# Performance work log

Measured on AMD Instinct MI355X. Metric: run time of the kernel, lower is better.

The kernel has to match this reference:

```python
import jax, jax.numpy as jnp
import numpy as np

N, E, NC, ES, NT, G = 200000, 500000, 150000, 350000, 100000, 1024
FN, FE, H, T = 133, 14, 128, 3


def _enc_params(key, prefix):
    ks = jax.random.split(key, 4)
    g = lambda k, shape, fan_in: jax.random.normal(k, shape, jnp.float32) / np.sqrt(fan_in).astype(np.float32)
    return {
        f"{prefix}_w_node": g(ks[0], (FN, H), FN),
        f"{prefix}_b_node": jnp.zeros((H,), jnp.float32),
        f"{prefix}_w_edge": g(ks[1], (FE, H), FE),
        f"{prefix}_b_edge": jnp.zeros((H,), jnp.float32),
        f"{prefix}_w_mp": g(ks[2], (T, H, H), H),
        f"{prefix}_b_mp": jnp.zeros((T, H), jnp.float32),
        f"{prefix}_w_out": g(ks[3], (H, H), H),
        f"{prefix}_b_out": jnp.zeros((H,), jnp.float32),
    }


def setup_inputs() -> dict:
    key = jax.random.key(0)
    k = lambda i: jax.random.fold_in(key, i)
    inp = {
        "x": jax.random.normal(k(0), (N, FN), jnp.float32),
        "node_weight": jax.random.uniform(k(1), (N,), jnp.float32),
        "edge_index": jax.random.randint(k(2), (2, E), 0, N),
        "edge_attr": jax.random.normal(k(3), (E, FE), jnp.float32),
        "edge_weight": jax.random.uniform(k(4), (E,), jnp.float32),
        "batch": jnp.sort(jax.random.randint(k(5), (N,), 0, G)),
        "context_nodes_mapper": jax.random.randint(k(6), (NC,), 0, N),
        "target_nodes_mapper": jax.random.randint(k(7), (NT,), 0, N),
        "combined_subgraphs": jax.random.randint(k(8), (2, ES), 0, NC),
        "subgraphs_edges_mapper": jax.random.randint(k(9), (ES,), 0, E),
        "context_edges_mask": jax.random.bernoulli(k(10), 0.7, (ES,)),
    }
    inp.update(_enc_params(k(11), "ctx"))
    inp.update(_enc_params(k(12), "tgt"))
    return inp


def wd_mpnn(x, src, dst, edge_attr, edge_weight, node_weight,
            w_node, b_node, w_edge, b_edge, w_mp, b_mp, w_out, b_out, n_nodes):
    # Weighted-edge node MPNN: gather source node states, combine with edge
    # embedding, scale by edge weight, scatter-sum onto destination nodes.
    h = jax.nn.relu(x @ w_node + b_node)                 # [n_nodes, H]
    eh = jax.nn.relu(edge_attr @ w_edge + b_edge)        # [n_edges, H]
    ew = edge_weight[:, None]
    for t in range(w_mp.shape[0]):
        msg = ew * (h[src] + eh)                         # gather [n_edges, H]
        agg = jax.ops.segment_sum(msg, dst, num_segments=n_nodes)
        h = jax.nn.relu(h + agg @ w_mp[t] + b_mp[t])
    return (h @ w_out + b_out) * node_weight[:, None]


def segment_mean(vals, seg, num_segments):
    s = jax.ops.segment_sum(vals, seg, num_segments=num_segments)
    c = jax.ops.segment_sum(jnp.ones((vals.shape[0],), vals.dtype), seg, num_segments=num_segments)
    return s / jnp.maximum(c, 1.0)[:, None]


def reference(x, node_weight, edge_index, edge_attr, edge_weight, batch,
              context_nodes_mapper, target_nodes_mapper, combined_subgraphs,
              subgraphs_edges_mapper, context_edges_mask,
              ctx_w_node, ctx_b_node, ctx_w_edge, ctx_b_edge, ctx_w_mp, ctx_b_mp, ctx_w_out, ctx_b_out,
              tgt_w_node, tgt_b_node, tgt_w_edge, tgt_b_edge, tgt_w_mp, tgt_b_mp, tgt_w_out, tgt_b_out):
    # --- context branch: gather subgraph node/edge features ---
    cx = x[context_nodes_mapper]                         # [NC, FN]
    cnw = node_weight[context_nodes_mapper]              # [NC]
    cea = edge_attr[subgraphs_edges_mapper]              # [ES, FE]
    # boolean edge mask folded into edge weights (messages scale linearly in
    # edge_weight, so zeroing masked edges == dropping them) -> jit friendly
    cew = edge_weight[subgraphs_edges_mapper] * context_edges_mask.astype(jnp.float32)
    csrc, cdst = combined_subgraphs[0], combined_subgraphs[1]
    ctx_nodes = wd_mpnn(cx, csrc, cdst, cea, cew, cnw,
                        ctx_w_node, ctx_b_node, ctx_w_edge, ctx_b_edge,
                        ctx_w_mp, ctx_b_mp, ctx_w_out, ctx_b_out, NC)
    ctx_emb = segment_mean(ctx_nodes, batch[context_nodes_mapper], G)   # [G, H]

    # --- target branch: full-graph encode, pool over target nodes ---
    full = wd_mpnn(x, edge_index[0], edge_index[1], edge_attr, edge_weight, node_weight,
                   tgt_w_node, tgt_b_node, tgt_w_edge, tgt_b_edge,
                   tgt_w_mp, tgt_b_mp, tgt_w_out, tgt_b_out, N)
    tgt_emb = segment_mean(full[target_nodes_mapper], batch[target_nodes_mapper], G)  # [G, H]

    return jnp.stack([ctx_emb, tgt_emb])                 # [2, G, H]
```

## Files before the change

kernel.cpp:

```cpp
#include <hip/hip_runtime.h>
#include <stdint.h>

#define H 128
#define FN 133
#define FE 14
#define NG 1024
#define APAD 132

__global__ void k_sniff(const unsigned int* __restrict__ w, int nwords, int* __restrict__ flag) {
    __shared__ int sawFloat, sawBig;
    if (threadIdx.x == 0) { sawFloat = 0; sawBig = 0; }
    __syncthreads();
    int f = 0, bg = 0;
    for (int i = threadIdx.x; i < nwords; i += blockDim.x) {
        unsigned int v = w[i];
        if (v == 0u || v == 1u) continue;
        if (v == 0x3F800000u) f = 1; else bg = 1;
    }
    if (f) atomicOr(&sawFloat, 1);
    if (bg) atomicOr(&sawBig, 1);
    __syncthreads();
    if (threadIdx.x == 0) *flag = sawBig ? 1 : (sawFloat ? 2 : 0);
}

__device__ __forceinline__ float mask_val(const void* mask, int mm, long e) {
    if (mm == 1)      return ((const unsigned char*)mask)[e] ? 1.f : 0.f;
    else if (mm == 2) return ((const float*)mask)[e];
    else              return ((const int*)mask)[e] ? 1.f : 0.f;
}

template<bool GATHER>
__global__ __launch_bounds__(256)
void k_gemm_enc(const float* __restrict__ x, const int* __restrict__ map, int nrows,
                const float* __restrict__ w, const float* __restrict__ bias,
                float* __restrict__ hout) {
    __shared__ float w_lds[32][H];
    __shared__ float a_lds[32][APAD];
    __shared__ int   m_lds[128];
    const int tid = threadIdx.x;
    const int rbase = blockIdx.x * 128;
    if (GATHER && tid < 128) {
        int row = rbase + tid;
        m_lds[tid] = (row < nrows) ? map[row] : 0;
    }
    const int tx = tid & 15, ty = tid >> 4;
    float acc[8][8] = {};
    for (int kc = 0; kc < 5; ++kc) {
        const int k0 = kc * 32;
        __syncthreads();
        for (int i = tid; i < 32 * 32; i += 256) {
            int kk = i >> 5, c4 = i & 31;
            float4 v = make_float4(0.f, 0.f, 0.f, 0.f);
            if (k0 + kk < FN)
                v = reinterpret_cast<const float4*>(w + (size_t)(k0 + kk) * H)[c4];
            *reinterpret_cast<float4*>(&w_lds[kk][c4 * 4]) = v;
        }
        for (int i = tid; i < 128 * 32; i += 256) {
            int r = i >> 5, kk = i & 31;
            int row = rbase + r;
            float v = 0.f;
            if (row < nrows && k0 + kk < FN) {
                int sr = GATHER ? m_lds[r] : row;
                v = x[(size_t)sr * FN + k0 + kk];
            }
            a_lds[kk][r] = v;
        }
        __syncthreads();
        #pragma unroll 4
        for (int k = 0; k < 32; ++k) {
            float4 a0 = *reinterpret_cast<const float4*>(&a_lds[k][ty * 8]);
            float4 a1 = *reinterpret_cast<const float4*>(&a_lds[k][ty * 8 + 4]);
            float4 w0 = *reinterpret_cast<const float4*>(&w_lds[k][tx * 8]);
            float4 w1 = *reinterpret_cast<const float4*>(&w_lds[k][tx * 8 + 4]);
            float aa[8] = {a0.x, a0.y, a0.z, a0.w, a1.x, a1.y, a1.z, a1.w};
            float ww[8] = {w0.x, w0.y, w0.z, w0.w, w1.x, w1.y, w1.z, w1.w};
            #pragma unroll
            for (int i2 = 0; i2 < 8; ++i2)
                #pragma unroll
                for (int j = 0; j < 8; ++j)
                    acc[i2][j] += aa[i2] * ww[j];
        }
    }
    float4 b0 = reinterpret_cast<const float4*>(bias)[tx * 2];
    float4 b1 = reinterpret_cast<const float4*>(bias)[tx * 2 + 1];
    float bb[8] = {b0.x, b0.y, b0.z, b0.w, b1.x, b1.y, b1.z, b1.w};
    #pragma unroll
    for (int i2 = 0; i2 < 8; ++i2) {
        int row = rbase + ty * 8 + i2;
        if (row < nrows) {
            float4 o0, o1;
            o0.x = fmaxf(acc[i2][0] + bb[0], 0.f); o0.y = fmaxf(acc[i2][1] + bb[1], 0.f);
            o0.z = fmaxf(acc[i2][2] + bb[2], 0.f); o0.w = fmaxf(acc[i2][3] + bb[3], 0.f);
            o1.x = fmaxf(acc[i2][4] + bb[4], 0.f); o1.y = fmaxf(acc[i2][5] + bb[5], 0.f);
            o1.z = fmaxf(acc[i2][6] + bb[6], 0.f); o1.w = fmaxf(acc[i2][7] + bb[7], 0.f);
            float* hp = hout + (size_t)row * H + tx * 8;
            *reinterpret_cast<float4*>(hp)     = o0;
            *reinterpret_cast<float4*>(hp + 4) = o1;
        }
    }
}

template<int MODE>
__global__ __launch_bounds__(256)
void k_hist(const int* __restrict__ dst, const float* __restrict__ edge_weight,
            const int* __restrict__ emap, const void* __restrict__ mask,
            const int* __restrict__ mmode_p, int* __restrict__ deg, int nedges) {
    int e = blockIdx.x * 256 + threadIdx.x;
    if (e >= nedges) return;
    int eo = MODE ? emap[e] : e;
    float w = edge_weight[eo];
    if (MODE) w *= mask_val(mask, *mmode_p, e);
    if (w != 0.f) atomicAdd(&deg[dst[e]], 1);
}

__global__ __launch_bounds__(256)
void k_scan1(const int* __restrict__ deg, int* __restrict__ off, int* __restrict__ bsum, int n) {
    __shared__ int tsum[256];
    const int tid = threadIdx.x;
    const int base = blockIdx.x * 1024;
    int local[4]; int s = 0;
    #pragma unroll
    for (int j = 0; j < 4; ++j) {
        int i = base + tid * 4 + j;
        local[j] = (i < n) ? deg[i] : 0;
        s += local[j];
    }
    tsum[tid] = s;
    __syncthreads();
    for (int d = 1; d < 256; d <<= 1) {
        int v = (tid >= d) ? tsum[tid - d] : 0;
        __syncthreads();
        tsum[tid] += v;
        __syncthreads();
    }
    int excl = tsum[tid] - s;
    #pragma unroll
    for (int j = 0; j < 4; ++j) {
        int i = base + tid * 4 + j;
        if (i < n) off[i] = excl;
        excl += local[j];
    }
    if (tid == 255) bsum[blockIdx.x] = tsum[255];
}

__global__ __launch_bounds__(256)
void k_scan2(int* __restrict__ bsum, int nb) {
    __shared__ int tsum[256];
    const int tid = threadIdx.x;
    int local[4]; int s = 0;
    #pragma unroll
    for (int j = 0; j < 4; ++j) {
        int i = tid * 4 + j;
        local[j] = (i < nb) ? bsum[i] : 0;
        s += local[j];
    }
    tsum[tid] = s;
    __syncthreads();
    for (int d = 1; d < 256; d <<= 1) {
        int v = (tid >= d) ? tsum[tid - d] : 0;
        __syncthreads();
        tsum[tid] += v;
        __syncthreads();
    }
    int excl = tsum[tid] - s;
    #pragma unroll
    for (int j = 0; j < 4; ++j) {
        int i = tid * 4 + j;
        if (i < nb) bsum[i] = excl;
        excl += local[j];
    }
}

__global__ __launch_bounds__(256)
void k_scan3(const int* __restrict__ bsum, int* __restrict__ off, int* __restrict__ cur, int n) {
    int i = blockIdx.x * 256 + threadIdx.x;
    if (i < n) {
        int o = off[i] + bsum[i >> 10];
        off[i] = o;
        cur[i] = o;
    }
}

template<int MODE>
__global__ __launch_bounds__(256)
void k_scatter(const int* __restrict__ src, const int* __restrict__ dst,
               const float* __restrict__ edge_weight,
               const int* __restrict__ emap, const void* __restrict__ mask,
               const int* __restrict__ mmode_p, int* __restrict__ cur,
               int2* __restrict__ epk, int2* __restrict__ epkh,
               int nedges) {
    int e = blockIdx.x * 256 + threadIdx.x;
    if (e >= nedges) return;
    int eo = MODE ? emap[e] : e;
    float w = edge_weight[eo];
    if (MODE) w *= mask_val(mask, *mmode_p, e);
    if (w != 0.f) {
        int pos = atomicAdd(&cur[dst[e]], 1);
        int wb = __float_as_int(w);
        epk[pos]  = make_int2(src[e], wb);
        epkh[pos] = make_int2(eo, wb);
    }
}

__global__ __launch_bounds__(256)
void k_eh_csr(const int* __restrict__ off, const int* __restrict__ deg,
              const int2* __restrict__ epkh,
              const float* __restrict__ edge_attr,
              const float* __restrict__ w_edge, const float* __restrict__ b_edge,
              float* __restrict__ aggeh, int nnodes) {
    __shared__ float we_lds[FE * H];
    __shared__ float be_lds[H];
    for (int i = threadIdx.x; i < FE * H; i += 256) we_lds[i] = w_edge[i];
    if (threadIdx.x < H) be_lds[threadIdx.x] = b_edge[threadIdx.x];
    __syncthreads();
    const int hw = threadIdx.x >> 5;
    const int ln = threadIdx.x & 31;
    const int c  = ln * 4;
    int v = blockIdx.x * 8 + hw;
    if (v >= nnodes) return;
    float4 acc = make_float4(0.f, 0.f, 0.f, 0.f);
    const int o = off[v], d = deg[v];
    const float4 bev = *reinterpret_cast<const float4*>(be_lds + c);
    for (int jb = 0; jb < d; jb += 32) {
        const int nn = min(32, d - jb);
        int2 meta = make_int2(0, 0);
        if (ln < nn) meta = epkh[o + jb + ln];
        const int me = meta.x;
        const float mw = __int_as_float(meta.y);
        for (int q = 0; q < nn; q += 2) {
            int   e0 = __shfl(me, q, 32);
            float w0 = __shfl(mw, q, 32);
            int   e1 = __shfl(me, q + 1, 32);
            float w1 = __shfl(mw, q + 1, 32);
            bool ok1 = (q + 1 < nn);
            if (!ok1) { e1 = e0; w1 = 0.f; }
            float a0 = (ln < FE) ? edge_attr[(size_t)e0 * FE + ln] : 0.f;
            float a1 = (ln < FE) ? edge_attr[(size_t)e1 * FE + ln] : 0.f;
            float4 eh0 = bev, eh1 = bev;
            #pragma unroll
            for (int k = 0; k < FE; ++k) {
                float f0 = __shfl(a0, k, 32);
                float f1 = __shfl(a1, k, 32);
                float4 wv = *reinterpret_cast<const float4*>(we_lds + k * H + c);
                eh0.x += f0 * wv.x; eh0.y += f0 * wv.y; eh0.z += f0 * wv.z; eh0.w += f0 * wv.w;
                eh1.x += f1 * wv.x; eh1.y += f1 * wv.y; eh1.z += f1 * wv.z; eh1.w += f1 * wv.w;
            }
            acc.x += w0 * fmaxf(eh0.x, 0.f) + w1 * fmaxf(eh1.x, 0.f);
            acc.y += w0 * fmaxf(eh0.y, 0.f) + w1 * fmaxf(eh1.y, 0.f);
            acc.z += w0 * fmaxf(eh0.z, 0.f) + w1 * fmaxf(eh1.z, 0.f);
            acc.w += w0 * fmaxf(eh0.w, 0.f) + w1 * fmaxf(eh1.w, 0.f);
        }
    }
    *reinterpret_cast<float4*>(aggeh + (size_t)v * H + c) = acc;
}

__global__ __launch_bounds__(256)
void k_msg_csr(const int* __restrict__ off, const int* __restrict__ deg,
               const int2* __restrict__ epk, const float* __restrict__ aggeh,
               const float* __restrict__ h, float* __restrict__ agg, int nnodes) {
    const int hw = threadIdx.x >> 5;
    const int c  = (threadIdx.x & 31) * 4;
    const int ln = threadIdx.x & 31;
    int v = blockIdx.x * 8 + hw;
    if (v >= nnodes) return;
    float4 acc = *reinterpret_cast<const float4*>(aggeh + (size_t)v * H + c);
    const int o = off[v], d = deg[v];
    for (int jb = 0; jb < d; jb += 32) {
        const int nn = min(32, d - jb);
        int2 meta = make_int2(0, 0);
        if (ln < nn) meta = epk[o + jb + ln];
        const int ms = meta.x;
        const float mw = __int_as_float(meta.y);
        for (int q = 0; q < nn; q += 4) {
            #pragma unroll
            for (int u = 0; u < 4; ++u) {
                int qq = q + u;
                int   s = __shfl(ms, qq, 32);
                float w = __shfl(mw, qq, 32);
                if (qq >= nn) { s = 0; w = 0.f; }
                float4 hv = *reinterpret_cast<const float4*>(h + (size_t)s * H + c);
                acc.x += w * hv.x; acc.y += w * hv.y;
                acc.z += w * hv.z; acc.w += w * hv.w;
            }
        }
    }
    *reinterpret_cast<float4*>(agg + (size_t)v * H + c) = acc;
}

__global__ __launch_bounds__(256)
void k_gemm_update(const float* __restrict__ agg, int nrows,
                   const float* __restrict__ w, const float* __restrict__ bias,
                   float* __restrict__ h) {
    __shared__ float w_lds[32][H];
    __shared__ float a_lds[32][APAD];
    const int tid = threadIdx.x;
    const int rbase = blockIdx.x * 128;
    const int tx = tid & 15, ty = tid >> 4;
    float acc[8][8] = {};
    for (int kc = 0; kc < 4; ++kc) {
        const int k0 = kc * 32;
        __syncthreads();
        for (int i = tid; i < 1024; i += 256) {
            int kk = i >> 5, c4 = i & 31;
            *reinterpret_cast<float4*>(&w_lds[kk][c4 * 4]) =
                reinterpret_cast<const float4*>(w + (size_t)(k0 + kk) * H)[c4];
        }
        for (int i = tid; i < 1024; i += 256) {
            int r = i >> 3, f = i & 7;
            int row = rbase + r;
            float4 v = make_float4(0.f, 0.f, 0.f, 0.f);
            if (row < nrows)
                v = reinterpret_cast<const float4*>(agg + (size_t)row * H + k0)[f];
            a_lds[f * 4 + 0][r] = v.x;
            a_lds[f * 4 + 1][r] = v.y;
            a_lds[f * 4 + 2][r] = v.z;
            a_lds[f * 4 + 3][r] = v.w;
        }
        __syncthreads();
        #pragma unroll 4
        for (int k = 0; k < 32; ++k) {
            float4 a0 = *reinterpret_cast<const float4*>(&a_lds[k][ty * 8]);
            float4 a1 = *reinterpret_cast<const float4*>(&a_lds[k][ty * 8 + 4]);
            float4 w0 = *reinterpret_cast<const float4*>(&w_lds[k][tx * 8]);
            float4 w1 = *reinterpret_cast<const float4*>(&w_lds[k][tx * 8 + 4]);
            float aa[8] = {a0.x, a0.y, a0.z, a0.w, a1.x, a1.y, a1.z, a1.w};
            float ww[8] = {w0.x, w0.y, w0.z, w0.w, w1.x, w1.y, w1.z, w1.w};
            #pragma unroll
            for (int i2 = 0; i2 < 8; ++i2)
                #pragma unroll
                for (int j = 0; j < 8; ++j)
                    acc[i2][j] += aa[i2] * ww[j];
        }
    }
    float4 b0 = reinterpret_cast<const float4*>(bias)[tx * 2];
    float4 b1 = reinterpret_cast<const float4*>(bias)[tx * 2 + 1];
    float bb[8] = {b0.x, b0.y, b0.z, b0.w, b1.x, b1.y, b1.z, b1.w};
    #pragma unroll
    for (int i2 = 0; i2 < 8; ++i2) {
        int row = rbase + ty * 8 + i2;
        if (row < nrows) {
            float* hp = h + (size_t)row * H + tx * 8;
            float4 h0 = *reinterpret_cast<const float4*>(hp);
            float4 h1 = *reinterpret_cast<const float4*>(hp + 4);
            float4 o0, o1;
            o0.x = fmaxf(h0.x + acc[i2][0] + bb[0], 0.f); o0.y = fmaxf(h0.y + acc[i2][1] + bb[1], 0.f);
            o0.z = fmaxf(h0.z + acc[i2][2] + bb[2], 0.f); o0.w = fmaxf(h0.w + acc[i2][3] + bb[3], 0.f);
            o1.x = fmaxf(h1.x + acc[i2][4] + bb[4], 0.f); o1.y = fmaxf(h1.y + acc[i2][5] + bb[5], 0.f);
            o1.z = fmaxf(h1.z + acc[i2][6] + bb[6], 0.f); o1.w = fmaxf(h1.w + acc[i2][7] + bb[7], 0.f);
            *reinterpret_cast<float4*>(hp)     = o0;
            *reinterpret_cast<float4*>(hp + 4) = o1;
        }
    }
}

__global__ __launch_bounds__(256)
void k_ghist(const int* __restrict__ rowmap, const int* __restrict__ batch,
             int* __restrict__ deg_g, int nrows) {
    int r = blockIdx.x * 256 + threadIdx.x;
    if (r < nrows) atomicAdd(&deg_g[batch[rowmap[r]]], 1);
}

__global__ __launch_bounds__(256)
void k_gscan(const int* __restrict__ deg, int* __restrict__ off, int* __restrict__ cur) {
    __shared__ int tsum[256];
    const int tid = threadIdx.x;
    int local[4]; int s = 0;
    #pragma unroll
    for (int j = 0; j < 4; ++j) { local[j] = deg[tid * 4 + j]; s += local[j]; }
    tsum[tid] = s;
    __syncthreads();
    for (int d = 1; d < 256; d <<= 1) {
        int v = (tid >= d) ? tsum[tid - d] : 0;
        __syncthreads();
        tsum[tid] += v;
        __syncthreads();
    }
    int excl = tsum[tid] - s;
    #pragma unroll
    for (int j = 0; j < 4; ++j) {
        off[tid * 4 + j] = excl;
        cur[tid * 4 + j] = excl;
        excl += local[j];
    }
}

template<bool GATHER>
__global__ __launch_bounds__(256)
void k_gscatter(const int* __restrict__ rowmap, const int* __restrict__ batch,
                const float* __restrict__ nodew, int* __restrict__ cur,
                int* __restrict__ prow, float* __restrict__ pnw, int nrows) {
    int r = blockIdx.x * 256 + threadIdx.x;
    if (r >= nrows) return;
    int oid = rowmap[r];
    int g = batch[oid];
    int pos = atomicAdd(&cur[g], 1);
    prow[pos] = GATHER ? oid : r;
    pnw[pos]  = nodew[oid];
}

__global__ __launch_bounds__(256)
void k_pool(const int* __restrict__ off_g, const int* __restrict__ deg_g,
            const int* __restrict__ prow, const float* __restrict__ pnw,
            const float* __restrict__ h,
            const float* __restrict__ w, const float* __restrict__ bias,
            float* __restrict__ outp) {
    __shared__ float s_lds[4][H];
    __shared__ float ssum[H];
    __shared__ float r_lds[2][H];
    __shared__ float cg_lds[4];
    const int g = blockIdx.x;
    const int o = off_g[g], cnt = deg_g[g];
    const int wv = threadIdx.x >> 6, lane = threadIdx.x & 63;
    float ax = 0.f, ay = 0.f, cg = 0.f;
    for (int i = wv; i < cnt; i += 4) {
        int hrow = prow[o + i];
        float nw = pnw[o + i];
        float2 v = *reinterpret_cast<const float2*>(h + (size_t)hrow * H + lane * 2);
        ax += nw * v.x; ay += nw * v.y; cg += nw;
    }
    s_lds[wv][lane * 2]     = ax;
    s_lds[wv][lane * 2 + 1] = ay;
    if (lane == 0) cg_lds[wv] = cg;
    __syncthreads();
    if (threadIdx.x < H)
        ssum[threadIdx.x] = s_lds[0][threadIdx.x] + s_lds[1][threadIdx.x]
                          + s_lds[2][threadIdx.x] + s_lds[3][threadIdx.x];
    __syncthreads();
    const int c = threadIdx.x & 127, kh = threadIdx.x >> 7;
    float p = 0.f;
    #pragma unroll 8
    for (int k = 0; k < 64; ++k)
        p += ssum[kh * 64 + k] * w[(size_t)(kh * 64 + k) * H + c];
    r_lds[kh][c] = p;
    __syncthreads();
    if (threadIdx.x < H) {
        float cga = cg_lds[0] + cg_lds[1] + cg_lds[2] + cg_lds[3];
        float val = r_lds[0][c] + r_lds[1][c] + bias[c] * cga;
        outp[(size_t)g * H + c] = val / fmaxf((float)cnt, 1.f);
    }
}

extern "C" void kernel_launch(void* const* d_in, const int* in_sizes, int n_in,
                              void* d_out, int out_size, void* d_ws, size_t ws_size,
                              hipStream_t stream) {
    (void)n_in; (void)out_size; (void)ws_size;
    const float* x           = (const float*)d_in[0];
    const float* node_weight = (const float*)d_in[1];
    const int*   edge_index  = (const int*)d_in[2];
    const float* edge_attr   = (const float*)d_in[3];
    const float* edge_weight = (const float*)d_in[4];
    const int*   batch       = (const int*)d_in[5];
    const int*   cnm         = (const int*)d_in[6];
    const int*   tnm         = (const int*)d_in[7];
    const int*   csub        = (const int*)d_in[8];
    const int*   sem         = (const int*)d_in[9];
    const void*  cmask       = d_in[10];

    const float* ctx_w_node = (const float*)d_in[11];
    const float* ctx_b_node = (const float*)d_in[12];
    const float* ctx_w_edge = (const float*)d_in[13];
    const float* ctx_b_edge = (const float*)d_in[14];
    const float* ctx_w_mp   = (const float*)d_in[15];
    const float* ctx_b_mp   = (const float*)d_in[16];
    const float* ctx_w_out  = (const float*)d_in[17];
    const float* ctx_b_out  = (const float*)d_in[18];
    const float* tgt_w_node = (const float*)d_in[19];
    const float* tgt_b_node = (const float*)d_in[20];
    const float* tgt_w_edge = (const float*)d_in[21];
    const float* tgt_b_edge = (const float*)d_in[22];
    const float* tgt_w_mp   = (const float*)d_in[23];
    const float* tgt_b_mp   = (const float*)d_in[24];
    const float* tgt_w_out  = (const float*)d_in[25];
    const float* tgt_b_out  = (const float*)d_in[26];

    const int N  = in_sizes[1];
    const int E  = in_sizes[4];
    const int NC = in_sizes[6];
    const int NT = in_sizes[7];
    const int ES = in_sizes[9];
    const int NMAX = (NT > NC) ? NT : NC;

    float* out = (float*)d_out;

    char* ws = (char*)d_ws;
    float* h      = (float*)ws;  ws += (size_t)N * H * sizeof(float);
    float* agg    = (float*)ws;  ws += (size_t)N * H * sizeof(float);
    float* aggeh  = (float*)ws;  ws += (size_t)N * H * sizeof(float);
    int2*  epk    = (int2*)ws;   ws += (size_t)E * sizeof(int2);
    int2*  epkh   = (int2*)ws;   ws += (size_t)E * sizeof(int2);
    int*   deg    = (int*)ws;    ws += (size_t)N * sizeof(int);
    int*   off    = (int*)ws;    ws += (size_t)N * sizeof(int);
    int*   cur    = (int*)ws;    ws += (size_t)N * sizeof(int);
    int*   bsum   = (int*)ws;    ws += 1024 * sizeof(int);
    int*   deg_g  = (int*)ws;    ws += NG * sizeof(int);
    int*   off_g  = (int*)ws;    ws += NG * sizeof(int);
    int*   cur_g  = (int*)ws;    ws += NG * sizeof(int);
    int*   prow   = (int*)ws;    ws += (size_t)NMAX * sizeof(int);
    float* pnw    = (float*)ws;  ws += (size_t)NMAX * sizeof(float);
    int*   flag   = (int*)ws;    ws += sizeof(int);

    int nwords = ES / 4; if (nwords > 8192) nwords = 8192;
    k_sniff<<<1, 256, 0, stream>>>((const unsigned int*)cmask, nwords, flag);

    {
        const int* fsrc = edge_index;
        const int* fdst = edge_index + E;
        hipMemsetAsync(deg, 0, (size_t)N * sizeof(int), stream);
        int egrid = (E + 255) / 256;
        k_hist<0><<<egrid, 256, 0, stream>>>(fdst, edge_weight, nullptr, nullptr, nullptr, deg, E);
        int nb1 = (N + 1023) / 1024;
        k_scan1<<<nb1, 256, 0, stream>>>(deg, off, bsum, N);
        k_scan2<<<1, 256, 0, stream>>>(bsum, nb1);
        k_scan3<<<(N + 255) / 256, 256, 0, stream>>>(bsum, off, cur, N);
        k_scatter<0><<<egrid, 256, 0, stream>>>(fsrc, fdst, edge_weight, nullptr, nullptr, nullptr,
                                                cur, epk, epkh, E);
        k_gemm_enc<false><<<(N + 127) / 128, 256, 0, stream>>>(x, nullptr, N, tgt_w_node, tgt_b_node, h);
        k_eh_csr<<<(N + 7) / 8, 256, 0, stream>>>(off, deg, epkh, edge_attr,
                                                  tgt_w_edge, tgt_b_edge, aggeh, N);
        for (int t = 0; t < 3; ++t) {
            k_msg_csr<<<(N + 7) / 8, 256, 0, stream>>>(off, deg, epk, aggeh, h, agg, N);
            k_gemm_update<<<(N + 127) / 128, 256, 0, stream>>>(agg, N,
                                                               tgt_w_mp + t * H * H, tgt_b_mp + t * H, h);
        }
        hipMemsetAsync(deg_g, 0, NG * sizeof(int), stream);
        k_ghist<<<(NT + 255) / 256, 256, 0, stream>>>(tnm, batch, deg_g, NT);
        k_gscan<<<1, 256, 0, stream>>>(deg_g, off_g, cur_g);
        k_gscatter<true><<<(NT + 255) / 256, 256, 0, stream>>>(tnm, batch, node_weight, cur_g, prow, pnw, NT);
        k_pool<<<NG, 256, 0, stream>>>(off_g, deg_g, prow, pnw, h, tgt_w_out, tgt_b_out,
                                       out + (size_t)NG * H);
    }

    {
        const int* csrc = csub;
        const int* cdst = csub + ES;
        hipMemsetAsync(deg, 0, (size_t)NC * sizeof(int), stream);
        int egrid = (ES + 255) / 256;
        k_hist<1><<<egrid, 256, 0, stream>>>(cdst, edge_weight, sem, cmask, flag, deg, ES);
        int nb1 = (NC + 1023) / 1024;
        k_scan1<<<nb1, 256, 0, stream>>>(deg, off, bsum, NC);
        k_scan2<<<1, 256, 0, stream>>>(bsum, nb1);
        k_scan3<<<(NC + 255) / 256, 256, 0, stream>>>(bsum, off, cur, NC);
        k_scatter<1><<<egrid, 256, 0, stream>>>(csrc, cdst, edge_weight, sem, cmask, flag,
                                                cur, epk, epkh, ES);
        k_gemm_enc<true><<<(NC + 127) / 128, 256, 0, stream>>>(x, cnm, NC, ctx_w_node, ctx_b_node, h);
        k_eh_csr<<<(NC + 7) / 8, 256, 0, stream>>>(off, deg, epkh, edge_attr,
                                                   ctx_w_edge, ctx_b_edge, aggeh, NC);
        for (int t = 0; t < 3; ++t) {
            k_msg_csr<<<(NC + 7) / 8, 256, 0, stream>>>(off, deg, epk, aggeh, h, agg, NC);
            k_gemm_update<<<(NC + 127) / 128, 256, 0, stream>>>(agg, NC,
                                                                ctx_w_mp + t * H * H, ctx_b_mp + t * H, h);
        }
        hipMemsetAsync(deg_g, 0, NG * sizeof(int), stream);
        k_ghist<<<(NC + 255) / 256, 256, 0, stream>>>(cnm, batch, deg_g, NC);
        k_gscan<<<1, 256, 0, stream>>>(deg_g, off_g, cur_g);
        k_gscatter<false><<<(NC + 255) / 256, 256, 0, stream>>>(cnm, batch, node_weight, cur_g, prow, pnw, NC);
        k_pool<<<NG, 256, 0, stream>>>(off_g, deg_g, prow, pnw, h, ctx_w_out, ctx_b_out, out);
    }
}
```

Before: 1.700 ms.

## Fuse message aggregation and update GEMM into one kernel with ping-pong h buffers

The separate CSR message-gather kernel and the dense update GEMM are merged into one kernel. Each block aggregates 64 destination rows into LDS and then multiplies them by the 128x128 weight, reading the weights straight from global/L1 instead of staging them in LDS. This removes the agg round-trip to global memory and one launch per layer. It needs double-buffered h arrays because the in-place update would race with the gathers of other blocks. The smaller 4x8 register tile and uncached weight reads may lower GEMM efficiency, and the irregular gather now shares occupancy with the GEMM phase.

```diff
diff --git a/kernel.cpp b/kernel.cpp
--- a/kernel.cpp
+++ b/kernel.cpp
@@ -255,91 +255,87 @@
 }
 
 __global__ __launch_bounds__(256)
-void k_msg_csr(const int* __restrict__ off, const int* __restrict__ deg,
-               const int2* __restrict__ epk, const float* __restrict__ aggeh,
-               const float* __restrict__ h, float* __restrict__ agg, int nnodes) {
-    const int hw = threadIdx.x >> 5;
-    const int c  = (threadIdx.x & 31) * 4;
-    const int ln = threadIdx.x & 31;
-    int v = blockIdx.x * 8 + hw;
-    if (v >= nnodes) return;
-    float4 acc = *reinterpret_cast<const float4*>(aggeh + (size_t)v * H + c);
-    const int o = off[v], d = deg[v];
-    for (int jb = 0; jb < d; jb += 32) {
-        const int nn = min(32, d - jb);
-        int2 meta = make_int2(0, 0);
-        if (ln < nn) meta = epk[o + jb + ln];
-        const int ms = meta.x;
-        const float mw = __int_as_float(meta.y);
-        for (int q = 0; q < nn; q += 4) {
+void k_mp_fused(const int* __restrict__ off, const int* __restrict__ deg,
+                const int2* __restrict__ epk, const float* __restrict__ aggeh,
+                const float* __restrict__ h_old,
+                const float* __restrict__ w_mp, const float* __restrict__ bias,
+                float* __restrict__ h_new, int nnodes) {
+    __shared__ float a_lds[64][APAD];
+    const int tid = threadIdx.x;
+    const int rbase = blockIdx.x * 64;
+    const int hw = tid >> 5, ln = tid & 31;
+    const int c = ln * 4;
+    #pragma unroll 1
+    for (int rr = 0; rr < 8; ++rr) {
+        const int r = hw * 8 + rr;
+        const int v = rbase + r;
+        float4 acc = make_float4(0.f, 0.f, 0.f, 0.f);
+        if (v < nnodes) {
+            acc = *reinterpret_cast<const float4*>(aggeh + (size_t)v * H + c);
+            const int o = off[v], d = deg[v];
+            for (int jb = 0; jb < d; jb += 32) {
+                const int nn = min(32, d - jb);
+                int2 meta = make_int2(0, 0);
+                if (ln < nn) meta = epk[o + jb + ln];
+                const int ms = meta.x;
+                const float mw = __int_as_float(meta.y);
+                for (int q = 0; q < nn; q += 4) {
+                    #pragma unroll
+                    for (int u = 0; u < 4; ++u) {
+                        int qq = q + u;
+                        int   s = __shfl(ms, qq, 32);
+                        float w = __shfl(mw, qq, 32);
+                        if (qq >= nn) { s = 0; w = 0.f; }
+                        float4 hv = *reinterpret_cast<const float4*>(h_old + (size_t)s * H + c);
+                        acc.x += w * hv.x; acc.y += w * hv.y;
+                        acc.z += w * hv.z; acc.w += w * hv.w;
+                    }
+                }
+            }
+        }
+        *reinterpret_cast<float4*>(&a_lds[r][c]) = acc;
+    }
+    __syncthreads();
+    const int tx = tid & 15, ty = tid >> 4;
+    float acc[4][8] = {};
+    #pragma unroll 2
+    for (int k = 0; k < H; k += 4) {
+        float4 a0 = *reinterpret_cast<const float4*>(&a_lds[ty * 4 + 0][k]);
+        float4 a1 = *reinterpret_cast<const float4*>(&a_lds[ty * 4 + 1][k]);
+        float4 a2 = *reinterpret_cast<const float4*>(&a_lds[ty * 4 + 2][k]);
+        float4 a3 = *reinterpret_cast<const float4*>(&a_lds[ty * 4 + 3][k]);
+        const float* wp = w_mp + (size_t)k * H + tx * 8;
+        float4 w00 = *reinterpret_cast<const float4*>(wp);
+        float4 w01 = *reinterpret_cast<const float4*>(wp + 4);
+        float4 w10 = *reinterpret_cast<const float4*>(wp + H);
+        float4 w11 = *reinterpret_cast<const float4*>(wp + H + 4);
+        float4 w20 = *reinterpret_cast<const float4*>(wp + 2 * H);
+        float4 w21 = *reinterpret_cast<const float4*>(wp + 2 * H + 4);
+        float4 w30 = *reinterpret_cast<const float4*>(wp + 3 * H);
+        float4 w31 = *reinterpret_cast<const float4*>(wp + 3 * H + 4);
+        float wk0[8] = {w00.x, w00.y, w00.z, w00.w, w01.x, w01.y, w01.z, w01.w};
+        float wk1[8] = {w10.x, w10.y, w10.z, w10.w, w11.x, w11.y, w11.z, w11.w};
+        float wk2[8] = {w20.x, w20.y, w20.z, w20.w, w21.x, w21.y, w21.z, w21.w};
+        float wk3[8] = {w30.x, w30.y, w30.z, w30.w, w31.x, w31.y, w31.z, w31.w};
+        float ak0[4] = {a0.x, a1.x, a2.x, a3.x};
+        float ak1[4] = {a0.y, a1.y, a2.y, a3.y};
+        float ak2[4] = {a0.z, a1.z, a2.z, a3.z};
+        float ak3[4] = {a0.w, a1.w, a2.w, a3.w};
+        #pragma unroll
+        for (int i2 = 0; i2 < 4; ++i2)
             #pragma unroll
-            for (int u = 0; u < 4; ++u) {
-                int qq = q + u;
-                int   s = __shfl(ms, qq, 32);
-                float w = __shfl(mw, qq, 32);
-                if (qq >= nn) { s = 0; w = 0.f; }
-                float4 hv = *reinterpret_cast<const float4*>(h + (size_t)s * H + c);
-                acc.x += w * hv.x; acc.y += w * hv.y;
-                acc.z += w * hv.z; acc.w += w * hv.w;
-            }
-        }
-    }
-    *reinterpret_cast<float4*>(agg + (size_t)v * H + c) = acc;
-}
-
-__global__ __launch_bounds__(256)
-void k_gemm_update(const float* __restrict__ agg, int nrows,
-                   const float* __restrict__ w, const float* __restrict__ bias,
-                   float* __restrict__ h) {
-    __shared__ float w_lds[32][H];
-    __shared__ float a_lds[32][APAD];
-    const int tid = threadIdx.x;
-    const int rbase = blockIdx.x * 128;
-    const int tx = tid & 15, ty = tid >> 4;
-    float acc[8][8] = {};
-    for (int kc = 0; kc < 4; ++kc) {
-        const int k0 = kc * 32;
-        __syncthreads();
-        for (int i = tid; i < 1024; i += 256) {
-            int kk = i >> 5, c4 = i & 31;
-            *reinterpret_cast<float4*>(&w_lds[kk][c4 * 4]) =
-                reinterpret_cast<const float4*>(w + (size_t)(k0 + kk) * H)[c4];
-        }
-        for (int i = tid; i < 1024; i += 256) {
-            int r = i >> 3, f = i & 7;
-            int row = rbase + r;
-            float4 v = make_float4(0.f, 0.f, 0.f, 0.f);
-            if (row < nrows)
-                v = reinterpret_cast<const float4*>(agg + (size_t)row * H + k0)[f];
-            a_lds[f * 4 + 0][r] = v.x;
-            a_lds[f * 4 + 1][r] = v.y;
-            a_lds[f * 4 + 2][r] = v.z;
-            a_lds[f * 4 + 3][r] = v.w;
-        }
-        __syncthreads();
-        #pragma unroll 4
-        for (int k = 0; k < 32; ++k) {
-            float4 a0 = *reinterpret_cast<const float4*>(&a_lds[k][ty * 8]);
-            float4 a1 = *reinterpret_cast<const float4*>(&a_lds[k][ty * 8 + 4]);
-            float4 w0 = *reinterpret_cast<const float4*>(&w_lds[k][tx * 8]);
-            float4 w1 = *reinterpret_cast<const float4*>(&w_lds[k][tx * 8 + 4]);
-            float aa[8] = {a0.x, a0.y, a0.z, a0.w, a1.x, a1.y, a1.z, a1.w};
-            float ww[8] = {w0.x, w0.y, w0.z, w0.w, w1.x, w1.y, w1.z, w1.w};
-            #pragma unroll
-            for (int i2 = 0; i2 < 8; ++i2)
-                #pragma unroll
-                for (int j = 0; j < 8; ++j)
-                    acc[i2][j] += aa[i2] * ww[j];
-        }
+            for (int j = 0; j < 8; ++j)
+                acc[i2][j] += ak0[i2] * wk0[j] + ak1[i2] * wk1[j]
+                            + ak2[i2] * wk2[j] + ak3[i2] * wk3[j];
     }
     float4 b0 = reinterpret_cast<const float4*>(bias)[tx * 2];
     float4 b1 = reinterpret_cast<const float4*>(bias)[tx * 2 + 1];
     float bb[8] = {b0.x, b0.y, b0.z, b0.w, b1.x, b1.y, b1.z, b1.w};
     #pragma unroll
-    for (int i2 = 0; i2 < 8; ++i2) {
-        int row = rbase + ty * 8 + i2;
-        if (row < nrows) {
-            float* hp = h + (size_t)row * H + tx * 8;
+    for (int i2 = 0; i2 < 4; ++i2) {
+        int row = rbase + ty * 4 + i2;
+        if (row < nnodes) {
+            const float* hp = h_old + (size_t)row * H + tx * 8;
             float4 h0 = *reinterpret_cast<const float4*>(hp);
             float4 h1 = *reinterpret_cast<const float4*>(hp + 4);
             float4 o0, o1;
@@ -347,8 +343,9 @@
             o0.z = fmaxf(h0.z + acc[i2][2] + bb[2], 0.f); o0.w = fmaxf(h0.w + acc[i2][3] + bb[3], 0.f);
             o1.x = fmaxf(h1.x + acc[i2][4] + bb[4], 0.f); o1.y = fmaxf(h1.y + acc[i2][5] + bb[5], 0.f);
             o1.z = fmaxf(h1.z + acc[i2][6] + bb[6], 0.f); o1.w = fmaxf(h1.w + acc[i2][7] + bb[7], 0.f);
-            *reinterpret_cast<float4*>(hp)     = o0;
-            *reinterpret_cast<float4*>(hp + 4) = o1;
+            float* op = h_new + (size_t)row * H + tx * 8;
+            *reinterpret_cast<float4*>(op)     = o0;
+            *reinterpret_cast<float4*>(op + 4) = o1;
         }
     }
 }
@@ -483,8 +480,8 @@
     float* out = (float*)d_out;
 
     char* ws = (char*)d_ws;
-    float* h      = (float*)ws;  ws += (size_t)N * H * sizeof(float);
-    float* agg    = (float*)ws;  ws += (size_t)N * H * sizeof(float);
+    float* hA     = (float*)ws;  ws += (size_t)N * H * sizeof(float);
+    float* hB     = (float*)ws;  ws += (size_t)N * H * sizeof(float);
     float* aggeh  = (float*)ws;  ws += (size_t)N * H * sizeof(float);
     int2*  epk    = (int2*)ws;   ws += (size_t)E * sizeof(int2);
     int2*  epkh   = (int2*)ws;   ws += (size_t)E * sizeof(int2);
@@ -514,19 +511,21 @@
         k_scan3<<<(N + 255) / 256, 256, 0, stream>>>(bsum, off, cur, N);
         k_scatter<0><<<egrid, 256, 0, stream>>>(fsrc, fdst, edge_weight, nullptr, nullptr, nullptr,
                                                 cur, epk, epkh, E);
-        k_gemm_enc<false><<<(N + 127) / 128, 256, 0, stream>>>(x, nullptr, N, tgt_w_node, tgt_b_node, h);
+        k_gemm_enc<false><<<(N + 127) / 128, 256, 0, stream>>>(x, nullptr, N, tgt_w_node, tgt_b_node, hA);
         k_eh_csr<<<(N + 7) / 8, 256, 0, stream>>>(off, deg, epkh, edge_attr,
                                                   tgt_w_edge, tgt_b_edge, aggeh, N);
+        float* hin = hA; float* hout = hB;
         for (int t = 0; t < 3; ++t) {
-            k_msg_csr<<<(N + 7) / 8, 256, 0, stream>>>(off, deg, epk, aggeh, h, agg, N);
-            k_gemm_update<<<(N + 127) / 128, 256, 0, stream>>>(agg, N,
-                                                               tgt_w_mp + t * H * H, tgt_b_mp + t * H, h);
+            k_mp_fused<<<(N + 63) / 64, 256, 0, stream>>>(off, deg, epk, aggeh, hin,
+                                                          tgt_w_mp + t * H * H, tgt_b_mp + t * H,
+                                                          hout, N);
+            float* tmp = hin; hin = hout; hout = tmp;
         }
         hipMemsetAsync(deg_g, 0, NG * sizeof(int), stream);
         k_ghist<<<(NT + 255) / 256, 256, 0, stream>>>(tnm, batch, deg_g, NT);
         k_gscan<<<1, 256, 0, stream>>>(deg_g, off_g, cur_g);
         k_gscatter<true><<<(NT + 255) / 256, 256, 0, stream>>>(tnm, batch, node_weight, cur_g, prow, pnw, NT);
-        k_pool<<<NG, 256, 0, stream>>>(off_g, deg_g, prow, pnw, h, tgt_w_out, tgt_b_out,
+        k_pool<<<NG, 256, 0, stream>>>(off_g, deg_g, prow, pnw, hin, tgt_w_out, tgt_b_out,
                                        out + (size_t)NG * H);
     }
 
@@ -542,18 +541,20 @@
         k_scan3<<<(NC + 255) / 256, 256, 0, stream>>>(bsum, off, cur, NC);
         k_scatter<1><<<egrid, 256, 0, stream>>>(csrc, cdst, edge_weight, sem, cmask, flag,
                                                 cur, epk, epkh, ES);
-        k_gemm_enc<true><<<(NC + 127) / 128, 256, 0, stream>>>(x, cnm, NC, ctx_w_node, ctx_b_node, h);
+        k_gemm_enc<true><<<(NC + 127) / 128, 256, 0, stream>>>(x, cnm, NC, ctx_w_node, ctx_b_node, hA);
         k_eh_csr<<<(NC + 7) / 8, 256, 0, stream>>>(off, deg, epkh, edge_attr,
                                                    ctx_w_edge, ctx_b_edge, aggeh, NC);
+        float* hin = hA; float* hout = hB;
         for (int t = 0; t < 3; ++t) {
-            k_msg_csr<<<(NC + 7) / 8, 256, 0, stream>>>(off, deg, epk, aggeh, h, agg, NC);
-            k_gemm_update<<<(NC + 127) / 128, 256, 0, stream>>>(agg, NC,
-                                                                ctx_w_mp + t * H * H, ctx_b_mp + t * H, h);
+            k_mp_fused<<<(NC + 63) / 64, 256, 0, stream>>>(off, deg, epk, aggeh, hin,
+                                                           ctx_w_mp + t * H * H, ctx_b_mp + t * H,
+                                                           hout, NC);
+            float* tmp = hin; hin = hout; hout = tmp;
         }
         hipMemsetAsync(deg_g, 0, NG * sizeof(int), stream);
         k_ghist<<<(NC + 255) / 256, 256, 0, stream>>>(cnm, batch, deg_g, NC);
         k_gscan<<<1, 256, 0, stream>>>(deg_g, off_g, cur_g);
         k_gscatter<false><<<(NC + 255) / 256, 256, 0, stream>>>(cnm, batch, node_weight, cur_g, prow, pnw, NC);
-        k_pool<<<NG, 256, 0, stream>>>(off_g, deg_g, prow, pnw, h, ctx_w_out, ctx_b_out, out);
-    }
-}
+        k_pool<<<NG, 256, 0, stream>>>(off_g, deg_g, prow, pnw, hin, ctx_w_out, ctx_b_out, out);
+    }
+}
```

Result: slower. 1.772 ms (+4.2%).

## Fuse edge-embedding aggregation with first message pass and remap GEMM column tiles

Applied to the files above, without the earlier changes.

The edge-embedding aggregation kernel now also gathers source node states for the first message-passing step, producing both agg and aggeh in one pass. This removes one CSR traversal and one launch per branch. Separately, both GEMM kernels change the per-thread column mapping from 8 contiguous columns to two 4-column chunks 64 apart, which is meant to reduce LDS bank conflicts and make global stores more coalesced. The A-tile LDS padding also changes from 132 to 133. The cost is extra register pressure in the fused kernel, which now holds the h gathers and two accumulators.

```diff
diff --git a/kernel.cpp b/kernel.cpp
--- a/kernel.cpp
+++ b/kernel.cpp
@@ -5,7 +5,7 @@
 #define FN 133
 #define FE 14
 #define NG 1024
-#define APAD 132
+#define APAD 133
 
 __global__ void k_sniff(const unsigned int* __restrict__ w, int nwords, int* __restrict__ flag) {
     __shared__ int sawFloat, sawBig;
@@ -70,8 +70,8 @@
         for (int k = 0; k < 32; ++k) {
             float4 a0 = *reinterpret_cast<const float4*>(&a_lds[k][ty * 8]);
             float4 a1 = *reinterpret_cast<const float4*>(&a_lds[k][ty * 8 + 4]);
-            float4 w0 = *reinterpret_cast<const float4*>(&w_lds[k][tx * 8]);
-            float4 w1 = *reinterpret_cast<const float4*>(&w_lds[k][tx * 8 + 4]);
+            float4 w0 = *reinterpret_cast<const float4*>(&w_lds[k][tx * 4]);
+            float4 w1 = *reinterpret_cast<const float4*>(&w_lds[k][64 + tx * 4]);
             float aa[8] = {a0.x, a0.y, a0.z, a0.w, a1.x, a1.y, a1.z, a1.w};
             float ww[8] = {w0.x, w0.y, w0.z, w0.w, w1.x, w1.y, w1.z, w1.w};
             #pragma unroll
@@ -81,8 +81,8 @@
                     acc[i2][j] += aa[i2] * ww[j];
         }
     }
-    float4 b0 = reinterpret_cast<const float4*>(bias)[tx * 2];
-    float4 b1 = reinterpret_cast<const float4*>(bias)[tx * 2 + 1];
+    float4 b0 = *reinterpret_cast<const float4*>(bias + tx * 4);
+    float4 b1 = *reinterpret_cast<const float4*>(bias + 64 + tx * 4);
     float bb[8] = {b0.x, b0.y, b0.z, b0.w, b1.x, b1.y, b1.z, b1.w};
     #pragma unroll
     for (int i2 = 0; i2 < 8; ++i2) {
@@ -93,9 +93,9 @@
             o0.z = fmaxf(acc[i2][2] + bb[2], 0.f); o0.w = fmaxf(acc[i2][3] + bb[3], 0.f);
             o1.x = fmaxf(acc[i2][4] + bb[4], 0.f); o1.y = fmaxf(acc[i2][5] + bb[5], 0.f);
             o1.z = fmaxf(acc[i2][6] + bb[6], 0.f); o1.w = fmaxf(acc[i2][7] + bb[7], 0.f);
-            float* hp = hout + (size_t)row * H + tx * 8;
-            *reinterpret_cast<float4*>(hp)     = o0;
-            *reinterpret_cast<float4*>(hp + 4) = o1;
+            float* hp = hout + (size_t)row * H + tx * 4;
+            *reinterpret_cast<float4*>(hp)      = o0;
+            *reinterpret_cast<float4*>(hp + 64) = o1;
         }
     }
 }
@@ -203,11 +203,12 @@
 }
 
 __global__ __launch_bounds__(256)
-void k_eh_csr(const int* __restrict__ off, const int* __restrict__ deg,
-              const int2* __restrict__ epkh,
+void k_msg_eh(const int* __restrict__ off, const int* __restrict__ deg,
+              const int2* __restrict__ epk, const int2* __restrict__ epkh,
               const float* __restrict__ edge_attr,
               const float* __restrict__ w_edge, const float* __restrict__ b_edge,
-              float* __restrict__ aggeh, int nnodes) {
+              const float* __restrict__ h,
+              float* __restrict__ agg, float* __restrict__ aggeh, int nnodes) {
     __shared__ float we_lds[FE * H];
     __shared__ float be_lds[H];
     for (int i = threadIdx.x; i < FE * H; i += 256) we_lds[i] = w_edge[i];
@@ -219,21 +220,26 @@
     int v = blockIdx.x * 8 + hw;
     if (v >= nnodes) return;
     float4 acc = make_float4(0.f, 0.f, 0.f, 0.f);
+    float4 aeh = make_float4(0.f, 0.f, 0.f, 0.f);
     const int o = off[v], d = deg[v];
     const float4 bev = *reinterpret_cast<const float4*>(be_lds + c);
     for (int jb = 0; jb < d; jb += 32) {
         const int nn = min(32, d - jb);
-        int2 meta = make_int2(0, 0);
-        if (ln < nn) meta = epkh[o + jb + ln];
-        const int me = meta.x;
-        const float mw = __int_as_float(meta.y);
+        int2 m1 = make_int2(0, 0), m2 = make_int2(0, 0);
+        if (ln < nn) { m1 = epk[o + jb + ln]; m2 = epkh[o + jb + ln]; }
+        const int msrc = m1.x;
+        const int meo  = m2.x;
+        const float mw = __int_as_float(m1.y);
         for (int q = 0; q < nn; q += 2) {
-            int   e0 = __shfl(me, q, 32);
-            float w0 = __shfl(mw, q, 32);
-            int   e1 = __shfl(me, q + 1, 32);
-            float w1 = __shfl(mw, q + 1, 32);
-            bool ok1 = (q + 1 < nn);
-            if (!ok1) { e1 = e0; w1 = 0.f; }
+            int   s0 = __shfl(msrc, q, 32);
+            int   e0 = __shfl(meo,  q, 32);
+            float w0 = __shfl(mw,   q, 32);
+            int   s1 = __shfl(msrc, q + 1, 32);
+            int   e1 = __shfl(meo,  q + 1, 32);
+            float w1 = __shfl(mw,   q + 1, 32);
+            if (q + 1 >= nn) { s1 = s0; e1 = e0; w1 = 0.f; }
+            float4 hv0 = *reinterpret_cast<const float4*>(h + (size_t)s0 * H + c);
+            float4 hv1 = *reinterpret_cast<const float4*>(h + (size_t)s1 * H + c);
             float a0 = (ln < FE) ? edge_attr[(size_t)e0 * FE + ln] : 0.f;
             float a1 = (ln < FE) ? edge_attr[(size_t)e1 * FE + ln] : 0.f;
             float4 eh0 = bev, eh1 = bev;
@@ -245,13 +251,20 @@
                 eh0.x += f0 * wv.x; eh0.y += f0 * wv.y; eh0.z += f0 * wv.z; eh0.w += f0 * wv.w;
                 eh1.x += f1 * wv.x; eh1.y += f1 * wv.y; eh1.z += f1 * wv.z; eh1.w += f1 * wv.w;
             }
-            acc.x += w0 * fmaxf(eh0.x, 0.f) + w1 * fmaxf(eh1.x, 0.f);
-            acc.y += w0 * fmaxf(eh0.y, 0.f) + w1 * fmaxf(eh1.y, 0.f);
-            acc.z += w0 * fmaxf(eh0.z, 0.f) + w1 * fmaxf(eh1.z, 0.f);
-            acc.w += w0 * fmaxf(eh0.w, 0.f) + w1 * fmaxf(eh1.w, 0.f);
-        }
-    }
-    *reinterpret_cast<float4*>(aggeh + (size_t)v * H + c) = acc;
+            float r0x = w0 * fmaxf(eh0.x, 0.f), r1x = w1 * fmaxf(eh1.x, 0.f);
+            float r0y = w0 * fmaxf(eh0.y, 0.f), r1y = w1 * fmaxf(eh1.y, 0.f);
+            float r0z = w0 * fmaxf(eh0.z, 0.f), r1z = w1 * fmaxf(eh1.z, 0.f);
+            float r0w = w0 * fmaxf(eh0.w, 0.f), r1w = w1 * fmaxf(eh1.w, 0.f);
+            aeh.x += r0x + r1x; aeh.y += r0y + r1y;
+            aeh.z += r0z + r1z; aeh.w += r0w + r1w;
+            acc.x += w0 * hv0.x + w1 * hv1.x + r0x + r1x;
+            acc.y += w0 * hv0.y + w1 * hv1.y + r0y + r1y;
+            acc.z += w0 * hv0.z + w1 * hv1.z + r0z + r1z;
+            acc.w += w0 * hv0.w + w1 * hv1.w + r0w + r1w;
+        }
+    }
+    *reinterpret_cast<float4*>(agg   + (size_t)v * H + c) = acc;
+    *reinterpret_cast<float4*>(aggeh + (size_t)v * H + c) = aeh;
 }
 
 __global__ __launch_bounds__(256)
@@ -259,8 +272,8 @@
                const int2* __restrict__ epk, const float* __restrict__ aggeh,
                const float* __restrict__ h, float* __restrict__ agg, int nnodes) {
     const int hw = threadIdx.x >> 5;
-    const int c  = (threadIdx.x & 31) * 4;
     const int ln = threadIdx.x & 31;
+    const int c  = ln * 4;
     int v = blockIdx.x * 8 + hw;
     if (v >= nnodes) return;
     float4 acc = *reinterpret_cast<const float4*>(aggeh + (size_t)v * H + c);
@@ -321,8 +334,8 @@
         for (int k = 0; k < 32; ++k) {
             float4 a0 = *reinterpret_cast<const float4*>(&a_lds[k][ty * 8]);
             float4 a1 = *reinterpret_cast<const float4*>(&a_lds[k][ty * 8 + 4]);
-            float4 w0 = *reinterpret_cast<const float4*>(&w_lds[k][tx * 8]);
-            float4 w1 = *reinterpret_cast<const float4*>(&w_lds[k][tx * 8 + 4]);
+            float4 w0 = *reinterpret_cast<const float4*>(&w_lds[k][tx * 4]);
+            float4 w1 = *reinterpret_cast<const float4*>(&w_lds[k][64 + tx * 4]);
             float aa[8] = {a0.x, a0.y, a0.z, a0.w, a1.x, a1.y, a1.z, a1.w};
             float ww[8] = {w0.x, w0.y, w0.z, w0.w, w1.x, w1.y, w1.z, w1.w};
             #pragma unroll
@@ -332,23 +345,23 @@
                     acc[i2][j] += aa[i2] * ww[j];
         }
     }
-    float4 b0 = reinterpret_cast<const float4*>(bias)[tx * 2];
-    float4 b1 = reinterpret_cast<const float4*>(bias)[tx * 2 + 1];
+    float4 b0 = *reinterpret_cast<const float4*>(bias + tx * 4);
+    float4 b1 = *reinterpret_cast<const float4*>(bias + 64 + tx * 4);
     float bb[8] = {b0.x, b0.y, b0.z, b0.w, b1.x, b1.y, b1.z, b1.w};
     #pragma unroll
     for (int i2 = 0; i2 < 8; ++i2) {
         int row = rbase + ty * 8 + i2;
         if (row < nrows) {
-            float* hp = h + (size_t)row * H + tx * 8;
+            float* hp = h + (size_t)row * H + tx * 4;
             float4 h0 = *reinterpret_cast<const float4*>(hp);
-            float4 h1 = *reinterpret_cast<const float4*>(hp + 4);
+            float4 h1 = *reinterpret_cast<const float4*>(hp + 64);
             float4 o0, o1;
             o0.x = fmaxf(h0.x + acc[i2][0] + bb[0], 0.f); o0.y = fmaxf(h0.y + acc[i2][1] + bb[1], 0.f);
             o0.z = fmaxf(h0.z + acc[i2][2] + bb[2], 0.f); o0.w = fmaxf(h0.w + acc[i2][3] + bb[3], 0.f);
             o1.x = fmaxf(h1.x + acc[i2][4] + bb[4], 0.f); o1.y = fmaxf(h1.y + acc[i2][5] + bb[5], 0.f);
             o1.z = fmaxf(h1.z + acc[i2][6] + bb[6], 0.f); o1.w = fmaxf(h1.w + acc[i2][7] + bb[7], 0.f);
-            *reinterpret_cast<float4*>(hp)     = o0;
-            *reinterpret_cast<float4*>(hp + 4) = o1;
+            *reinterpret_cast<float4*>(hp)      = o0;
+            *reinterpret_cast<float4*>(hp + 64) = o1;
         }
     }
 }
@@ -515,9 +528,10 @@
         k_scatter<0><<<egrid, 256, 0, stream>>>(fsrc, fdst, edge_weight, nullptr, nullptr, nullptr,
                                                 cur, epk, epkh, E);
         k_gemm_enc<false><<<(N + 127) / 128, 256, 0, stream>>>(x, nullptr, N, tgt_w_node, tgt_b_node, h);
-        k_eh_csr<<<(N + 7) / 8, 256, 0, stream>>>(off, deg, epkh, edge_attr,
-                                                  tgt_w_edge, tgt_b_edge, aggeh, N);
-        for (int t = 0; t < 3; ++t) {
+        k_msg_eh<<<(N + 7) / 8, 256, 0, stream>>>(off, deg, epk, epkh, edge_attr,
+                                                  tgt_w_edge, tgt_b_edge, h, agg, aggeh, N);
+        k_gemm_update<<<(N + 127) / 128, 256, 0, stream>>>(agg, N, tgt_w_mp, tgt_b_mp, h);
+        for (int t = 1; t < 3; ++t) {
             k_msg_csr<<<(N + 7) / 8, 256, 0, stream>>>(off, deg, epk, aggeh, h, agg, N);
             k_gemm_update<<<(N + 127) / 128, 256, 0, stream>>>(agg, N,
                                                                tgt_w_mp + t * H * H, tgt_b_mp + t * H, h);
@@ -543,9 +557,10 @@
         k_scatter<1><<<egrid, 256, 0, stream>>>(csrc, cdst, edge_weight, sem, cmask, flag,
                                                 cur, epk, epkh, ES);
         k_gemm_enc<true><<<(NC + 127) / 128, 256, 0, stream>>>(x, cnm, NC, ctx_w_node, ctx_b_node, h);
-        k_eh_csr<<<(NC + 7) / 8, 256, 0, stream>>>(off, deg, epkh, edge_attr,
-                                                   ctx_w_edge, ctx_b_edge, aggeh, NC);
-        for (int t = 0; t < 3; ++t) {
+        k_msg_eh<<<(NC + 7) / 8, 256, 0, stream>>>(off, deg, epk, epkh, edge_attr,
+                                                   ctx_w_edge, ctx_b_edge, h, agg, aggeh, NC);
+        k_gemm_update<<<(NC + 127) / 128, 256, 0, stream>>>(agg, NC, ctx_w_mp, ctx_b_mp, h);
+        for (int t = 1; t < 3; ++t) {
             k_msg_csr<<<(NC + 7) / 8, 256, 0, stream>>>(off, deg, epk, aggeh, h, agg, NC);
             k_gemm_update<<<(NC + 127) / 128, 256, 0, stream>>>(agg, NC,
                                                                 ctx_w_mp + t * H * H, ctx_b_mp + t * H, h);
```

Result: faster. 1.636 ms (-3.7%).
